# Kernel tuning notes

Hardware: AMD Instinct MI355X
Metric: run time of the kernel (lower is better)

Reference implementation:

```python
import jax, jax.numpy as jnp
import numpy as np

B, T, C, E, H, K = 4, 2048, 1024, 8, 2048, 2


def setup_inputs() -> dict:
    key = jax.random.key(0)
    k1, k2, k3, k4 = jax.random.split(key, 4)
    x = jax.random.normal(k1, (B, T, C), jnp.float32)
    router_w = jax.random.normal(k2, (E, C), jnp.float32) * 0.02
    fc_w = jax.random.normal(k3, (E, H, C), jnp.float32) * 0.02
    proj_w = jax.random.normal(k4, (E, C, H), jnp.float32) * 0.02
    return {"x": x, "router_w": router_w, "fc_w": fc_w, "proj_w": proj_w}


def reference(x, router_w, fc_w, proj_w):
    Bb, Tt, Cc = x.shape
    Ee = router_w.shape[0]
    k = K
    N = Bb * Tt
    x_flat = x.reshape(N, Cc)

    # Router: linear -> softmax -> top-k, renormalize
    scores = x_flat @ router_w.T                       # [N, E]
    routing_weights = jax.nn.softmax(scores, axis=-1)  # [N, E]
    top_w, top_idx = jax.lax.top_k(routing_weights, k) # [N, k]
    top_w = top_w / (top_w.sum(-1, keepdims=True) + 1e-10)

    flat_expert_ids = top_idx.reshape(-1)              # [N*k]
    flat_weights = top_w.reshape(-1)
    flat_token_ids = jnp.repeat(jnp.arange(N), k)

    # Stable sort by expert id (token permute)
    order = jnp.argsort(flat_expert_ids, stable=True)
    se = flat_expert_ids[order]
    st = flat_token_ids[order]
    sw = flat_weights[order]
    permuted_x = x_flat[st]                            # [N*k, C]

    tokens_per_expert = jnp.bincount(flat_expert_ids, length=Ee)
    offsets = jnp.concatenate([jnp.zeros((1,), tokens_per_expert.dtype),
                               jnp.cumsum(tokens_per_expert)[:-1]])
    pos_in_expert = jnp.arange(N * k) - offsets[se]
    capacity = 2 * N * k // Ee
    flat_batch_idx = se * capacity + pos_in_expert
    valid = pos_in_expert < capacity

    # Scatter tokens into capacity-padded per-expert batches (overflow dropped)
    scatter_idx = jnp.where(valid, flat_batch_idx, Ee * capacity)  # OOB => drop
    batched_x = jnp.zeros((Ee * capacity, Cc), x.dtype).at[scatter_idx].set(
        permuted_x, mode='drop')
    batched_x = batched_x.reshape(Ee, capacity, Cc)

    # Grouped GEMM: fc -> relu^2 -> proj
    hidden = jnp.square(jax.nn.relu(jnp.einsum('eic,ehc->eih', batched_x, fc_w)))
    batched_out = jnp.einsum('eih,ech->eic', hidden, proj_w).reshape(Ee * capacity, Cc)

    # Gather back, weight, scatter-add combine
    gathered = batched_out[jnp.where(valid, flat_batch_idx, 0)]
    weighted = gathered * jnp.where(valid, sw, 0.0)[:, None]
    output = jnp.zeros((N, Cc), x.dtype).at[st].add(weighted)
    return output.reshape(Bb, Tt, Cc), routing_weights.reshape(Bb, Tt, Ee)
```

## Files before the change

### kernel.cpp

```cpp
#include <hip/hip_runtime.h>
#include <hip/hip_bf16.h>
#include <stdint.h>

#define NB 4
#define NTT 2048
#define NC 1024
#define NE 8
#define NH 2048
#define NKK 2
#define NTOK (NB * NTT)
#define CAP (2 * NTOK * NKK / NE)

typedef __hip_bfloat16 bf16;
typedef __attribute__((ext_vector_type(8))) short short8;
typedef __attribute__((ext_vector_type(4))) short short4v;
typedef __attribute__((ext_vector_type(4))) float floatx4;
typedef __attribute__((ext_vector_type(2))) float floatx2;

typedef const __attribute__((address_space(1))) void* gas_ptr;
typedef __attribute__((address_space(3))) void* las_ptr;

static __device__ __forceinline__ void async_copy16(const void* g, void* l) {
  __builtin_amdgcn_global_load_lds((gas_ptr)g, (las_ptr)l, 16, 0, 0);
}

static __device__ __forceinline__ unsigned short f2b(float f) {
  bf16 h = __float2bfloat16(f);
  unsigned short u;
  __builtin_memcpy(&u, &h, 2);
  return u;
}
static __device__ __forceinline__ int iclamp(int v, int lo, int hi) {
  return v < lo ? lo : (v > hi ? hi : v);
}

__global__ __launch_bounds__(256) void zero_out_kernel(float* __restrict__ out) {
  const size_t i = ((size_t)blockIdx.x * 256 + threadIdx.x) * 4;
  floatx4 z = {0.f, 0.f, 0.f, 0.f};
  *reinterpret_cast<floatx4*>(out + i) = z;
}

__global__ __launch_bounds__(256) void cvt_kernel(const float* __restrict__ src,
                                                  bf16* __restrict__ dst) {
  const size_t i = ((size_t)blockIdx.x * 256 + threadIdx.x) * 8;
  const floatx4 a = *reinterpret_cast<const floatx4*>(src + i);
  const floatx4 b = *reinterpret_cast<const floatx4*>(src + i + 4);
  short8 r;
  r[0] = (short)f2b(a[0]); r[1] = (short)f2b(a[1]);
  r[2] = (short)f2b(a[2]); r[3] = (short)f2b(a[3]);
  r[4] = (short)f2b(b[0]); r[5] = (short)f2b(b[1]);
  r[6] = (short)f2b(b[2]); r[7] = (short)f2b(b[3]);
  *reinterpret_cast<short8*>(dst + i) = r;
}

__global__ __launch_bounds__(256) void router_kernel(
    const float* __restrict__ x, const float* __restrict__ rw,
    float* __restrict__ rw_out, int* __restrict__ epair,
    float* __restrict__ wpair, bf16* __restrict__ xb) {
  __shared__ float rws[NE * NC];
  const int tid = threadIdx.x;
  {
    const floatx4* rw4 = reinterpret_cast<const floatx4*>(rw);
    floatx4* rwl4 = reinterpret_cast<floatx4*>(rws);
#pragma unroll
    for (int i = 0; i < 8; ++i) rwl4[i * 256 + tid] = rw4[i * 256 + tid];
  }
  __syncthreads();

  const int wave = tid >> 6;
  const int lane = tid & 63;
  const int t = blockIdx.x * 4 + wave;
  const floatx4* xr4 = reinterpret_cast<const floatx4*>(x + (size_t)t * NC);
  const floatx4* rwl4 = reinterpret_cast<const floatx4*>(rws);
  bf16* xbr = xb + (size_t)t * NC;

  floatx4 xv[4];
#pragma unroll
  for (int i = 0; i < 4; ++i) xv[i] = xr4[i * 64 + lane];

#pragma unroll
  for (int i = 0; i < 4; ++i) {
    const int idx = i * 64 + lane;
    short4v o;
    o[0] = (short)f2b(xv[i][0]); o[1] = (short)f2b(xv[i][1]);
    o[2] = (short)f2b(xv[i][2]); o[3] = (short)f2b(xv[i][3]);
    *reinterpret_cast<short4v*>(xbr + idx * 4) = o;
  }

  float acc[NE];
#pragma unroll
  for (int e = 0; e < NE; ++e) acc[e] = 0.f;
#pragma unroll
  for (int i = 0; i < 4; ++i) {
    const int idx = i * 64 + lane;
#pragma unroll
    for (int e = 0; e < NE; ++e) {
      const floatx4 wv = rwl4[e * 256 + idx];
      acc[e] = fmaf(xv[i][0], wv[0], acc[e]);
      acc[e] = fmaf(xv[i][1], wv[1], acc[e]);
      acc[e] = fmaf(xv[i][2], wv[2], acc[e]);
      acc[e] = fmaf(xv[i][3], wv[3], acc[e]);
    }
  }
#pragma unroll
  for (int e = 0; e < NE; ++e) {
#pragma unroll
    for (int off = 32; off; off >>= 1) acc[e] += __shfl_xor(acc[e], off, 64);
  }

  float m = acc[0];
#pragma unroll
  for (int e = 1; e < NE; ++e) m = fmaxf(m, acc[e]);
  float p[NE];
  float s = 0.f;
#pragma unroll
  for (int e = 0; e < NE; ++e) {
    p[e] = __expf(acc[e] - m);
    s += p[e];
  }
  const float inv = 1.f / s;
#pragma unroll
  for (int e = 0; e < NE; ++e) p[e] *= inv;

  if (lane < NE) rw_out[(size_t)t * NE + lane] = p[lane];

  if (lane == 0) {
    int i0 = 0;
    float v0 = p[0];
    int i1 = -1;
    float v1 = -1.f;
#pragma unroll
    for (int e = 1; e < NE; ++e) {
      if (p[e] > v0) {
        v1 = v0; i1 = i0;
        v0 = p[e]; i0 = e;
      } else if (p[e] > v1) {
        v1 = p[e]; i1 = e;
      }
    }
    i0 = iclamp(i0, 0, NE - 1);
    i1 = iclamp(i1, 0, NE - 1);
    const float denom = v0 + v1 + 1e-10f;
    epair[t] = i0 | (i1 << 16);
    floatx2 wv;
    wv[0] = v0 / denom;
    wv[1] = v1 / denom;
    *reinterpret_cast<floatx2*>(wpair + 2 * t) = wv;
  }
}

__global__ __launch_bounds__(256) void build_kernel(
    const int* __restrict__ epair, const float* __restrict__ wpair,
    int* __restrict__ cnt, int* __restrict__ tok, float* __restrict__ wslot) {
  const int e = blockIdx.x;
  const int tid = threadIdx.x;
  const int lane = tid & 63;
  const int wave = tid >> 6;
  constexpr int TPT = NTOK / 256;
  const int t0 = tid * TPT;

  int pe[TPT];
#pragma unroll
  for (int i = 0; i < TPT; i += 4) {
    const int4 v = *reinterpret_cast<const int4*>(epair + t0 + i);
    pe[i] = v.x; pe[i + 1] = v.y; pe[i + 2] = v.z; pe[i + 3] = v.w;
  }
  int c = 0;
#pragma unroll
  for (int i = 0; i < TPT; ++i)
    c += (((pe[i] & 0xffff) == e) ? 1 : 0) + (((pe[i] >> 16) == e) ? 1 : 0);

  int incl = c;
#pragma unroll
  for (int off = 1; off < 64; off <<= 1) {
    const int up = __shfl_up(incl, off, 64);
    if (lane >= off) incl += up;
  }
  __shared__ int wsum[4];
  if (lane == 63) wsum[wave] = incl;
  __syncthreads();
  int base = incl - c;
#pragma unroll
  for (int w = 0; w < 4; ++w)
    if (w < wave) base += wsum[w];
  if (tid == 255) cnt[e] = base + c;

#pragma unroll
  for (int i = 0; i < TPT; ++i) {
    const int t = t0 + i;
    if ((pe[i] & 0xffff) == e) {
      if (base < CAP) {
        tok[e * CAP + base] = t;
        wslot[e * CAP + base] = wpair[2 * t];
      }
      ++base;
    }
    if ((pe[i] >> 16) == e) {
      if (base < CAP) {
        tok[e * CAP + base] = t;
        wslot[e * CAP + base] = wpair[2 * t + 1];
      }
      ++base;
    }
  }
}

template <bool FC>
__global__ __launch_bounds__(512, 2) void gemm_moe(
    const bf16* __restrict__ Axb, const bf16* __restrict__ Ah,
    const bf16* __restrict__ Bw, bf16* __restrict__ Oh,
    float* __restrict__ Oo, const int* __restrict__ cnt,
    const int* __restrict__ tok, const float* __restrict__ wslot,
    int rowOffset, int mch) {
  constexpr int Kd = FC ? NC : NH;
  constexpr int Nd = FC ? NH : NC;
  const int e = blockIdx.z;
  const int Me = iclamp(cnt[e], 0, CAP);
  const int rowBase = rowOffset + blockIdx.y * 256;
  if (rowBase >= Me) return;
  const int colBase = blockIdx.x * 256;

  const bf16* __restrict__ Be = Bw + (size_t)e * Nd * Kd;
  const bf16* __restrict__ Ahc = Ah + (size_t)e * mch * NH;

  __shared__ bf16 As[2][256 * 64];
  __shared__ bf16 Bs[2][256 * 64];

  const int tid = threadIdx.x;
  const int lane = tid & 63;
  const int wid = tid >> 6;
  const int wm = wid & 1;
  const int wn = wid >> 1;
  const int ml = lane & 15;
  const int quad = lane >> 4;

  const bf16* ga[4];
  const bf16* gb[4];
  int lofs[4];
#pragma unroll
  for (int it = 0; it < 4; ++it) {
    const int sidx = it * 512 + tid;
    const int r = sidx >> 3;
    const int pc = sidx & 7;
    const int lc = pc ^ (r & 7);
    if (FC) {
      const int grow = rowBase + r;
      const int tk = (grow < Me) ? tok[e * CAP + grow] : 0;
      const int arow = iclamp(tk, 0, NTOK - 1);
      ga[it] = Axb + (size_t)arow * NC + lc * 8;
    } else {
      int grow = rowBase + r;
      if (grow > Me - 1) grow = Me - 1;
      const int arow = iclamp(grow - rowOffset, 0, mch - 1);
      ga[it] = Ahc + (size_t)arow * NH + lc * 8;
    }
    gb[it] = Be + (size_t)(colBase + r) * Kd + lc * 8;
    lofs[it] = sidx * 8;
  }

  floatx4 acc[8][4];
#pragma unroll
  for (int mt = 0; mt < 8; ++mt)
#pragma unroll
    for (int nt = 0; nt < 4; ++nt) acc[mt][nt] = floatx4{0.f, 0.f, 0.f, 0.f};

  int aoff[8], boff[4];
#pragma unroll
  for (int mt = 0; mt < 8; ++mt) {
    const int ra = wm * 128 + mt * 16 + ml;
    aoff[mt] = (ra * 8 + (quad ^ (ra & 7))) * 8;
  }
#pragma unroll
  for (int nt = 0; nt < 4; ++nt) {
    const int rb = wn * 64 + nt * 16 + ml;
    boff[nt] = (rb * 8 + (quad ^ (rb & 7))) * 8;
  }

#pragma unroll
  for (int it = 0; it < 4; ++it) async_copy16(ga[it], &As[0][lofs[it]]);
#pragma unroll
  for (int it = 0; it < 4; ++it) async_copy16(gb[it], &Bs[0][lofs[it]]);

  const int nkb = Kd >> 6;
  for (int t = 0; t < nkb; ++t) {
    const int b = t & 1;
    if (t + 1 < nkb) {
      const int k0 = (t + 1) << 6;
#pragma unroll
      for (int it = 0; it < 4; ++it)
        async_copy16(ga[it] + k0, &As[b ^ 1][lofs[it]]);
#pragma unroll
      for (int it = 0; it < 4; ++it)
        async_copy16(gb[it] + k0, &Bs[b ^ 1][lofs[it]]);
      asm volatile("s_waitcnt vmcnt(8)" ::: "memory");
    } else {
      asm volatile("s_waitcnt vmcnt(0)" ::: "memory");
    }
    __builtin_amdgcn_s_barrier();
    __builtin_amdgcn_sched_barrier(0);
#pragma unroll
    for (int kk = 0; kk < 2; ++kk) {
      const int x = kk * 32;
      short8 af[8], bf[4];
#pragma unroll
      for (int mt = 0; mt < 8; ++mt)
        af[mt] = *reinterpret_cast<const short8*>(&As[b][aoff[mt] ^ x]);
#pragma unroll
      for (int nt = 0; nt < 4; ++nt)
        bf[nt] = *reinterpret_cast<const short8*>(&Bs[b][boff[nt] ^ x]);
      asm volatile("s_waitcnt lgkmcnt(0)" ::: "memory");
      __builtin_amdgcn_sched_barrier(0);
      __builtin_amdgcn_s_setprio(1);
#pragma unroll
      for (int mt = 0; mt < 8; ++mt)
#pragma unroll
        for (int nt = 0; nt < 4; ++nt)
          acc[mt][nt] = __builtin_amdgcn_mfma_f32_16x16x32_bf16(
              af[mt], bf[nt], acc[mt][nt], 0, 0, 0);
      __builtin_amdgcn_s_setprio(0);
    }
    __builtin_amdgcn_s_barrier();
    __builtin_amdgcn_sched_barrier(0);
  }

  if (FC) {
    bf16* __restrict__ O = Oh + (size_t)e * mch * NH;
    const int rlBase = rowBase - rowOffset;
#pragma unroll
    for (int mt = 0; mt < 8; ++mt) {
      const int rl = wm * 128 + mt * 16 + quad * 4;
#pragma unroll
      for (int nt = 0; nt < 4; ++nt) {
        const int cc = colBase + wn * 64 + nt * 16 + ml;
        const floatx4 v = acc[mt][nt];
#pragma unroll
        for (int rg = 0; rg < 4; ++rg) {
          if (rowBase + rl + rg < Me) {
            float f = fmaxf(v[rg], 0.f);
            f = f * f;
            O[(size_t)(rlBase + rl + rg) * NH + cc] = __float2bfloat16(f);
          }
        }
      }
    }
  } else {
#pragma unroll
    for (int mt = 0; mt < 8; ++mt) {
      const int rl = wm * 128 + mt * 16 + quad * 4;
#pragma unroll
      for (int rg = 0; rg < 4; ++rg) {
        const int re = rowBase + rl + rg;
        if (re < Me) {
          const int t = iclamp(tok[e * CAP + re], 0, NTOK - 1);
          const float w = wslot[e * CAP + re];
#pragma unroll
          for (int nt = 0; nt < 4; ++nt) {
            const int cc = colBase + wn * 64 + nt * 16 + ml;
            atomicAdd(Oo + (size_t)t * NC + cc, w * acc[mt][nt][rg]);
          }
        }
      }
    }
  }
}

extern "C" void kernel_launch(void* const* d_in, const int* in_sizes, int n_in,
                              void* d_out, int out_size, void* d_ws,
                              size_t ws_size, hipStream_t stream) {
  const float* x = (const float*)d_in[0];
  const float* rw = (const float*)d_in[1];
  const float* fcw = (const float*)d_in[2];
  const float* pjw = (const float*)d_in[3];
  float* out = (float*)d_out;
  float* rw_out = out + (size_t)NTOK * NC;

  char* ws = (char*)d_ws;
  int* cnt = (int*)ws;
  int* tok = (int*)(ws + 256);
  float* wslot = (float*)(ws + 256 + 131072);
  int* epair = (int*)(ws + 262400);
  float* wpair = (float*)(ws + 262400 + 32768);
  bf16* xb = (bf16*)(ws + 360704);
  bf16* fcwb = (bf16*)(ws + 360704 + 16777216);
  bf16* pjwb = (bf16*)(ws + 360704 + 16777216 + 33554432);
  const size_t fixed = 360704 + 16777216 + 2 * 33554432;
  bf16* hidden = (bf16*)(ws + fixed);
  (void)in_sizes; (void)n_in; (void)out_size;

  int mch = 256;
  for (int cand = CAP; cand >= 256; cand >>= 1) {
    const size_t need = fixed + (size_t)NE * cand * NH * 2;
    if (need <= ws_size) { mch = cand; break; }
  }

  zero_out_kernel<<<NTOK * NC / 1024, 256, 0, stream>>>(out);
  cvt_kernel<<<NE * NH * NC / 2048, 256, 0, stream>>>(fcw, fcwb);
  cvt_kernel<<<NE * NC * NH / 2048, 256, 0, stream>>>(pjw, pjwb);
  router_kernel<<<NTOK / 4, 256, 0, stream>>>(x, rw, rw_out, epair, wpair, xb);
  build_kernel<<<NE, 256, 0, stream>>>(epair, wpair, cnt, tok, wslot);

  for (int c = 0; c < CAP / mch; ++c) {
    gemm_moe<true><<<dim3(NH / 256, mch / 256, NE), 512, 0, stream>>>(
        xb, hidden, fcwb, hidden, out, cnt, tok, wslot, c * mch, mch);
    gemm_moe<false><<<dim3(NC / 256, mch / 256, NE), 512, 0, stream>>>(
        xb, hidden, pjwb, hidden, out, cnt, tok, wslot, c * mch, mch);
  }
}
```

Baseline: 486.5 us.

## Split GEMM k-step into four phases with interleaved prefetch and flatten grid

```diff
diff --git a/kernel.cpp b/kernel.cpp
--- a/kernel.cpp
+++ b/kernel.cpp
@@ -214,11 +214,18 @@
     int rowOffset, int mch) {
   constexpr int Kd = FC ? NC : NH;
   constexpr int Nd = FC ? NH : NC;
-  const int e = blockIdx.z;
+  constexpr int NXB = Nd / 256;
+
+  const int bid = blockIdx.x;
+  const int e = bid & 7;
+  const int rest = bid >> 3;
+  const int xb_ = rest % NXB;
+  const int yb_ = rest / NXB;
+
   const int Me = iclamp(cnt[e], 0, CAP);
-  const int rowBase = rowOffset + blockIdx.y * 256;
+  const int rowBase = rowOffset + yb_ * 256;
   if (rowBase >= Me) return;
-  const int colBase = blockIdx.x * 256;
+  const int colBase = xb_ * 256;
 
   const bf16* __restrict__ Be = Bw + (size_t)e * Nd * Kd;
   const bf16* __restrict__ Ahc = Ah + (size_t)e * mch * NH;
@@ -280,47 +287,52 @@
   for (int it = 0; it < 4; ++it) async_copy16(ga[it], &As[0][lofs[it]]);
 #pragma unroll
   for (int it = 0; it < 4; ++it) async_copy16(gb[it], &Bs[0][lofs[it]]);
+  asm volatile("s_waitcnt vmcnt(0)" ::: "memory");
+  __builtin_amdgcn_s_barrier();
 
   const int nkb = Kd >> 6;
-  for (int t = 0; t < nkb; ++t) {
-    const int b = t & 1;
-    if (t + 1 < nkb) {
-      const int k0 = (t + 1) << 6;
-#pragma unroll
-      for (int it = 0; it < 4; ++it)
-        async_copy16(ga[it] + k0, &As[b ^ 1][lofs[it]]);
-#pragma unroll
-      for (int it = 0; it < 4; ++it)
-        async_copy16(gb[it] + k0, &Bs[b ^ 1][lofs[it]]);
-      asm volatile("s_waitcnt vmcnt(8)" ::: "memory");
-    } else {
-      asm volatile("s_waitcnt vmcnt(0)" ::: "memory");
-    }
-    __builtin_amdgcn_s_barrier();
-    __builtin_amdgcn_sched_barrier(0);
-#pragma unroll
-    for (int kk = 0; kk < 2; ++kk) {
-      const int x = kk * 32;
-      short8 af[8], bf[4];
-#pragma unroll
-      for (int mt = 0; mt < 8; ++mt)
-        af[mt] = *reinterpret_cast<const short8*>(&As[b][aoff[mt] ^ x]);
-#pragma unroll
-      for (int nt = 0; nt < 4; ++nt)
-        bf[nt] = *reinterpret_cast<const short8*>(&Bs[b][boff[nt] ^ x]);
+  short8 af[8];
+  for (int kt = 0; kt < nkb; ++kt) {
+    const int b = kt & 1;
+    const bf16* __restrict__ Ab = As[b];
+    const bf16* __restrict__ Bb = Bs[b];
+#pragma unroll
+    for (int ph = 0; ph < 4; ++ph) {
+      const int kk = ph >> 1;
+      const int nh = ph & 1;
+      const int xr = kk * 32;
+      if (nh == 0) {
+#pragma unroll
+        for (int mt = 0; mt < 8; ++mt)
+          af[mt] = *reinterpret_cast<const short8*>(&Ab[aoff[mt] ^ xr]);
+      }
+      short8 b0 = *reinterpret_cast<const short8*>(&Bb[boff[2 * nh] ^ xr]);
+      short8 b1 = *reinterpret_cast<const short8*>(&Bb[boff[2 * nh + 1] ^ xr]);
+      if (ph == 0 && kt + 1 < nkb) {
+        const int k0 = (kt + 1) << 6;
+#pragma unroll
+        for (int it = 0; it < 4; ++it)
+          async_copy16(ga[it] + k0, &As[b ^ 1][lofs[it]]);
+#pragma unroll
+        for (int it = 0; it < 4; ++it)
+          async_copy16(gb[it] + k0, &Bs[b ^ 1][lofs[it]]);
+      }
+      if (ph == 3) asm volatile("s_waitcnt vmcnt(0)" ::: "memory");
+      __builtin_amdgcn_s_barrier();
       asm volatile("s_waitcnt lgkmcnt(0)" ::: "memory");
       __builtin_amdgcn_sched_barrier(0);
       __builtin_amdgcn_s_setprio(1);
 #pragma unroll
-      for (int mt = 0; mt < 8; ++mt)
-#pragma unroll
-        for (int nt = 0; nt < 4; ++nt)
-          acc[mt][nt] = __builtin_amdgcn_mfma_f32_16x16x32_bf16(
-              af[mt], bf[nt], acc[mt][nt], 0, 0, 0);
+      for (int mt = 0; mt < 8; ++mt) {
+        acc[mt][2 * nh] = __builtin_amdgcn_mfma_f32_16x16x32_bf16(
+            af[mt], b0, acc[mt][2 * nh], 0, 0, 0);
+        acc[mt][2 * nh + 1] = __builtin_amdgcn_mfma_f32_16x16x32_bf16(
+            af[mt], b1, acc[mt][2 * nh + 1], 0, 0, 0);
+      }
       __builtin_amdgcn_s_setprio(0);
-    }
-    __builtin_amdgcn_s_barrier();
-    __builtin_amdgcn_sched_barrier(0);
+      __builtin_amdgcn_s_barrier();
+      __builtin_amdgcn_sched_barrier(0);
+    }
   }
 
   if (FC) {
@@ -400,9 +412,9 @@
   build_kernel<<<NE, 256, 0, stream>>>(epair, wpair, cnt, tok, wslot);
 
   for (int c = 0; c < CAP / mch; ++c) {
-    gemm_moe<true><<<dim3(NH / 256, mch / 256, NE), 512, 0, stream>>>(
+    gemm_moe<true><<<NE * (NH / 256) * (mch / 256), 512, 0, stream>>>(
         xb, hidden, fcwb, hidden, out, cnt, tok, wslot, c * mch, mch);
-    gemm_moe<false><<<dim3(NC / 256, mch / 256, NE), 512, 0, stream>>>(
+    gemm_moe<false><<<NE * (NC / 256) * (mch / 256), 512, 0, stream>>>(
         xb, hidden, pjwb, hidden, out, cnt, tok, wslot, c * mch, mch);
   }
 }
```

Result: no change. 495.8 us (+1.9%).
